# Kernel optimization log

Hardware: AMD Instinct MI355X
Metric: run time of the kernel (lower is better)

Reference implementation:

```python
import jax, jax.numpy as jnp
import numpy as np
import math

EMBED = 1024
HEADS = 16
DHEAD = 64
B, S = 2, 2048


def setup_inputs() -> dict:
    key = jax.random.key(0)
    k1, k2, k3, k4 = jax.random.split(key, 4)
    qs = jax.random.normal(k1, (B, S, EMBED), dtype=jnp.float32)
    # causal mask, broadcast over batch (mask==0 positions are masked out)
    mask = jnp.broadcast_to(jnp.tril(jnp.ones((S, S), dtype=jnp.int32)), (B, S, S))
    # torch Linear(embed, 3*H*D, bias=False): y = x @ W^T; store transposed [E, 3HD]
    Wqkv = jax.random.normal(k2, (EMBED, 3 * HEADS * DHEAD), dtype=jnp.float32) / math.sqrt(EMBED)
    Wout = jax.random.normal(k3, (HEADS * DHEAD, EMBED), dtype=jnp.float32) / math.sqrt(HEADS * DHEAD)
    bout = jax.random.normal(k4, (EMBED,), dtype=jnp.float32) * 0.01
    return {"qs": qs, "mask": mask, "Wqkv": Wqkv, "Wout": Wout, "bout": bout}


def reference(qs, mask, Wqkv, Wout, bout):
    b, s, _ = qs.shape
    # fused QKV projection -> (B, S, 3H, D), split into q/k/v chunks of H heads
    qkv = (qs @ Wqkv).reshape(b, s, 3 * HEADS, DHEAD)
    q, k, v = qkv[:, :, :HEADS], qkv[:, :, HEADS:2 * HEADS], qkv[:, :, 2 * HEADS:]
    # scores: (B, H, Sq, Sk)
    scores = jnp.einsum("bqhd,bkhd->bhqk", q, k) / math.sqrt(DHEAD)
    scores = jnp.where(mask[:, None, :, :] == 0, jnp.float32(-1e9), scores)
    attn = jax.nn.softmax(scores, axis=-1)
    out = jnp.einsum("bhqk,bkhd->bqhd", attn, v).reshape(b, s, HEADS * DHEAD)
    return out @ Wout + bout
```

## Files before the change

kernel.cpp:

```cpp
#include <hip/hip_runtime.h>
#include <hip/hip_bf16.h>
#include <stdint.h>


typedef __attribute__((ext_vector_type(8))) short  short8;
typedef __attribute__((ext_vector_type(4))) short  short4v;
typedef __attribute__((ext_vector_type(4))) float  float4v;

#define SOFTMAX_BIAS 17.3123405f

__device__ __forceinline__ unsigned short f2bf(float f) {
  unsigned int u = __builtin_bit_cast(unsigned int, f);
  u += 0x7fffu + ((u >> 16) & 1u);
  return (unsigned short)(u >> 16);
}
__device__ __forceinline__ unsigned short f2bf_trunc(float f) {
  return (unsigned short)(__builtin_bit_cast(unsigned int, f) >> 16);
}
__device__ __forceinline__ float bf2f(unsigned short s) {
  unsigned int u = ((unsigned int)s) << 16;
  return __builtin_bit_cast(float, u);
}

__device__ __forceinline__ void async_copy16(const void* g, void* l) {
  __builtin_amdgcn_global_load_lds(
      (__attribute__((address_space(1))) unsigned int*)g,
      (__attribute__((address_space(3))) unsigned int*)l, 16, 0, 0);
}

__global__ void prep_kernel(const float* __restrict__ qs,
                            const float* __restrict__ Wqkv,
                            const float* __restrict__ Wout,
                            unsigned short* __restrict__ qs_bf,
                            unsigned short* __restrict__ WqkvT,
                            unsigned short* __restrict__ WoutT) {
  __shared__ float tbuf[32][33];
  const int blk = blockIdx.x, tid = threadIdx.x;
  if (blk < 4096) {
    int i = (blk * 256 + tid) * 4;
    float4v v = *(const float4v*)(qs + i);
    short4v o;
    o[0] = (short)f2bf(v[0]); o[1] = (short)f2bf(v[1]);
    o[2] = (short)f2bf(v[2]); o[3] = (short)f2bf(v[3]);
    *(short4v*)(qs_bf + i) = o;
  } else {
    const float* W; unsigned short* Wt; int N, t;
    if (blk < 4096 + 3072) { W = Wqkv; Wt = WqkvT; N = 3072; t = blk - 4096; }
    else                   { W = Wout; Wt = WoutT; N = 1024; t = blk - 7168; }
    const int tilesx = N >> 5;
    const int n0 = (t % tilesx) * 32, k0 = (t / tilesx) * 32;
    const int x = tid & 31, y = tid >> 5;
#pragma unroll
    for (int i = 0; i < 4; ++i)
      tbuf[y + i * 8][x] = W[(size_t)(k0 + y + i * 8) * N + n0 + x];
    __syncthreads();
#pragma unroll
    for (int i = 0; i < 4; ++i)
      Wt[(size_t)(n0 + y + i * 8) * 1024 + k0 + x] = f2bf(tbuf[x][y + i * 8]);
  }
}

__device__ __forceinline__ void gemm_bt_core(const unsigned short* __restrict__ A,
                                             const unsigned short* __restrict__ Bt,
                                             int m0, int n0,
                                             short* As, short* Bs,
                                             float4v (&acc)[4][4],
                                             int wm, int wn, int l15, int quad,
                                             int tid) {
  for (int k0 = 0; k0 < 1024; k0 += 32) {
    __syncthreads();
#pragma unroll
    for (int i = 0; i < 2; ++i) {
      int u = i * 256 + tid;
      int r = u >> 2, cpw = u & 3;
      int c = cpw ^ ((r >> 1) & 3);
      async_copy16(A  + (size_t)(m0 + r) * 1024 + k0 + c * 8, As + u * 8);
      async_copy16(Bt + (size_t)(n0 + r) * 1024 + k0 + c * 8, Bs + u * 8);
    }
    __syncthreads();

    short8 af[4], bfv[4];
#pragma unroll
    for (int t = 0; t < 4; ++t) {
      int ra = wm * 64 + t * 16 + l15;
      af[t]  = *(const short8*)(As + (ra * 4 + (quad ^ ((ra >> 1) & 3))) * 8);
      int rb = wn * 64 + t * 16 + l15;
      bfv[t] = *(const short8*)(Bs + (rb * 4 + (quad ^ ((rb >> 1) & 3))) * 8);
    }
#pragma unroll
    for (int mt = 0; mt < 4; ++mt)
#pragma unroll
      for (int nt = 0; nt < 4; ++nt)
        acc[mt][nt] = __builtin_amdgcn_mfma_f32_16x16x32_bf16(
            af[mt], bfv[nt], acc[mt][nt], 0, 0, 0);
  }
}

__global__ __launch_bounds__(256, 3)
void gemm_qkv_kernel(const unsigned short* __restrict__ Aq,
                     const unsigned short* __restrict__ Bt,
                     unsigned short* __restrict__ Qb,
                     unsigned short* __restrict__ Kb,
                     unsigned short* __restrict__ Vb) {
  __shared__ short As[128 * 32];
  __shared__ short Bs[128 * 32];
  const int tid = threadIdx.x, lane = tid & 63, w = tid >> 6;
  const int wm = w & 1, wn = w >> 1, l15 = lane & 15, quad = lane >> 4;
  const int m0 = blockIdx.x * 128, n0 = blockIdx.y * 128;

  float4v acc[4][4];
#pragma unroll
  for (int i = 0; i < 4; ++i)
#pragma unroll
    for (int j = 0; j < 4; ++j) acc[i][j] = (float4v)0.0f;

  gemm_bt_core(Aq, Bt, m0, n0, As, Bs, acc, wm, wn, l15, quad, tid);

#pragma unroll
  for (int nt = 0; nt < 4; ++nt) {
    int gn = n0 + wn * 64 + nt * 16 + l15;
    int j = gn >> 6, d = gn & 63;
    int g = j >> 4, h = j & 15;
#pragma unroll
    for (int mt = 0; mt < 4; ++mt) {
#pragma unroll
      for (int r = 0; r < 4; ++r) {
        int gm = m0 + wm * 64 + mt * 16 + quad * 4 + r;
        int b = gm >> 11, s = gm & 2047;
        float v = acc[mt][nt][r];
        if (g == 0)
          Qb[(((size_t)(b * 16 + h) * 2048 + s) << 6) + d] = f2bf(v * 0.18033688f);
        else if (g == 1)
          Kb[(((size_t)(b * 16 + h) * 2048 + s) << 6) + d] = f2bf(v);
        else
          Vb[(((size_t)(b * 16 + h) * 64 + d) << 11) + s] = f2bf(v);
      }
    }
  }
}

__global__ __launch_bounds__(256, 2)
void flash_attn_kernel(const unsigned short* __restrict__ Qb,
                       const unsigned short* __restrict__ Kb,
                       const unsigned short* __restrict__ Vb,
                       unsigned short* __restrict__ Pp0,
                       unsigned short* __restrict__ Pp1,
                       float* __restrict__ lws) {
  __shared__ unsigned short Kt[128 * 64];
  __shared__ unsigned short Vt[64 * 128];
  __shared__ unsigned short Pl[4][32 * 80];

  const int tid = threadIdx.x, lane = tid & 63, w = tid >> 6;
  const int l15 = lane & 15, quad = lane >> 4;
  const int qt = 15 - (blockIdx.x >> 1);
  const int half = blockIdx.x & 1;
  const int bh = blockIdx.y;
  const int bb = bh >> 4, h = bh & 15;

  const int n = qt + 1, nh0 = (n + 1) >> 1;
  const int kt_lo = half ? nh0 : 0;
  const int kt_hi = half ? n : nh0;

  const unsigned short* Qg = Qb + (size_t)bh * 2048 * 64;
  const unsigned short* Kg = Kb + (size_t)bh * 2048 * 64;
  const unsigned short* Vg = Vb + (size_t)bh * 64 * 2048;
  unsigned short* Pw = &Pl[w][0];

  const int qb0 = qt * 128 + w * 32;

  short8 qf[2][2];
#pragma unroll
  for (int nt = 0; nt < 2; ++nt)
#pragma unroll
    for (int kc = 0; kc < 2; ++kc)
      qf[nt][kc] = *(const short8*)(Qg + (size_t)(qb0 + nt * 16 + l15) * 64 +
                                    kc * 32 + quad * 8);

  float l_s[2] = {0.0f, 0.0f};
  float4v o[4][2];
#pragma unroll
  for (int i = 0; i < 4; ++i) { o[i][0] = (float4v)0.0f; o[i][1] = (float4v)0.0f; }

  for (int kt = kt_lo; kt < kt_hi; ++kt) {
    const int kb = kt * 128;
    __syncthreads();
#pragma unroll
    for (int i = 0; i < 4; ++i) {
      int u = i * 256 + tid;
      int r = u >> 3, cp = u & 7;
      async_copy16(Kg + (size_t)(kb + r) * 64 + (cp ^ (r & 7)) * 8, Kt + u * 8);
      int r2 = u >> 4, cp2 = u & 15;
      async_copy16(Vg + (size_t)r2 * 2048 + kb + (cp2 ^ (r2 & 15)) * 8, Vt + u * 8);
    }
    __syncthreads();

    float4v st[8][2];
#pragma unroll
    for (int mt = 0; mt < 8; ++mt) {
      st[mt][0] = (float4v)(-SOFTMAX_BIAS);
      st[mt][1] = (float4v)(-SOFTMAX_BIAS);
      int key = mt * 16 + l15;
#pragma unroll
      for (int kc = 0; kc < 2; ++kc) {
        int cp = (kc * 4 + quad) ^ (key & 7);
        short8 a = *(const short8*)(Kt + key * 64 + cp * 8);
        st[mt][0] = __builtin_amdgcn_mfma_f32_16x16x32_bf16(a, qf[0][kc], st[mt][0], 0, 0, 0);
        st[mt][1] = __builtin_amdgcn_mfma_f32_16x16x32_bf16(a, qf[1][kc], st[mt][1], 0, 0, 0);
      }
    }

    if (kt == qt) {
#pragma unroll
      for (int nt = 0; nt < 2; ++nt) {
        int qg = qb0 + nt * 16 + l15;
#pragma unroll
        for (int mt = 0; mt < 8; ++mt)
#pragma unroll
          for (int r = 0; r < 4; ++r) {
            int keyg = kb + mt * 16 + quad * 4 + r;
            if (keyg > qg) st[mt][nt][r] = -1e5f;
          }
      }
    }

#pragma unroll
    for (int nt = 0; nt < 2; ++nt) {
      float sum = 0.0f;
#pragma unroll
      for (int mt = 0; mt < 8; ++mt)
#pragma unroll
        for (int r = 0; r < 4; ++r) {
          float p = __builtin_amdgcn_exp2f(st[mt][nt][r]);
          st[mt][nt][r] = p;
          sum += p;
        }
      sum += __shfl_xor(sum, 16);
      sum += __shfl_xor(sum, 32);
      l_s[nt] += sum;
    }

#pragma unroll
    for (int hf = 0; hf < 2; ++hf) {
#pragma unroll
      for (int nt = 0; nt < 2; ++nt) {
        int ql = nt * 16 + l15;
        unsigned short* prow = Pw + ql * 80;
#pragma unroll
        for (int mtl = 0; mtl < 4; ++mtl) {
          int mt = hf * 4 + mtl;
          short4v pk;
          pk[0] = (short)f2bf_trunc(st[mt][nt][0]);
          pk[1] = (short)f2bf_trunc(st[mt][nt][1]);
          pk[2] = (short)f2bf_trunc(st[mt][nt][2]);
          pk[3] = (short)f2bf_trunc(st[mt][nt][3]);
          int cp = (mtl * 2 + (quad >> 1)) ^ (l15 & 7);
          *(short4v*)(prow + cp * 8 + (quad & 1) * 4) = pk;
        }
      }
#pragma unroll
      for (int kcl = 0; kcl < 2; ++kcl) {
        int kcg = hf * 2 + kcl;
        short8 pb[2];
#pragma unroll
        for (int nt = 0; nt < 2; ++nt) {
          int ql = nt * 16 + l15;
          int cp = (kcl * 4 + quad) ^ (l15 & 7);
          pb[nt] = *(const short8*)(Pw + ql * 80 + cp * 8);
        }
#pragma unroll
        for (int mtd = 0; mtd < 4; ++mtd) {
          int d = mtd * 16 + l15;
          int cp2 = (kcg * 4 + quad) ^ (d & 15);
          short8 a = *(const short8*)(Vt + d * 128 + cp2 * 8);
          o[mtd][0] = __builtin_amdgcn_mfma_f32_16x16x32_bf16(a, pb[0], o[mtd][0], 0, 0, 0);
          o[mtd][1] = __builtin_amdgcn_mfma_f32_16x16x32_bf16(a, pb[1], o[mtd][1], 0, 0, 0);
        }
      }
    }
  }

  unsigned short* Pp = half ? Pp1 : Pp0;
#pragma unroll
  for (int nt = 0; nt < 2; ++nt) {
    int qg = qb0 + nt * 16 + l15;
    if (quad == 0) lws[half * 65536 + bh * 2048 + qg] = l_s[nt];
#pragma unroll
    for (int mtd = 0; mtd < 4; ++mtd) {
      short4v pk;
      pk[0] = (short)f2bf(o[mtd][nt][0]);
      pk[1] = (short)f2bf(o[mtd][nt][1]);
      pk[2] = (short)f2bf(o[mtd][nt][2]);
      pk[3] = (short)f2bf(o[mtd][nt][3]);
      *(short4v*)(Pp + (size_t)(bb * 2048 + qg) * 1024 + h * 64 + mtd * 16 +
                  quad * 4) = pk;
    }
  }
}

__global__ void combine_kernel(const unsigned short* __restrict__ P0,
                               unsigned short* __restrict__ P1,
                               const float* __restrict__ lws) {
  int idx = (blockIdx.x * 256 + threadIdx.x) * 8;
  int t = idx >> 10, c = idx & 1023;
  int bh = (t >> 11) * 16 + (c >> 6);
  int q = t & 2047;
  float inv = 1.0f / (lws[bh * 2048 + q] + lws[65536 + bh * 2048 + q]);
  short8 a = *(const short8*)(P0 + idx);
  short8 b = *(const short8*)(P1 + idx);
  short8 r;
#pragma unroll
  for (int j = 0; j < 8; ++j)
    r[j] = (short)f2bf((bf2f((unsigned short)a[j]) +
                        bf2f((unsigned short)b[j])) * inv);
  *(short8*)(P1 + idx) = r;
}

__global__ __launch_bounds__(256, 3)
void gemm_out_kernel(const unsigned short* __restrict__ Aq,
                     const unsigned short* __restrict__ Bt,
                     const float* __restrict__ bout,
                     float* __restrict__ out) {
  __shared__ short As[64 * 32];
  __shared__ short Bs[128 * 32];
  const int tid = threadIdx.x, lane = tid & 63, w = tid >> 6;
  const int wm = w & 1, wn = w >> 1, l15 = lane & 15, quad = lane >> 4;
  const int m0 = blockIdx.x * 64, n0 = blockIdx.y * 128;

  float4v acc[2][4];
#pragma unroll
  for (int i = 0; i < 2; ++i)
#pragma unroll
    for (int j = 0; j < 4; ++j) acc[i][j] = (float4v)0.0f;

  for (int k0 = 0; k0 < 1024; k0 += 32) {
    __syncthreads();
    {
      int u = tid;
      int r = u >> 2, cpw = u & 3;
      int c = cpw ^ ((r >> 1) & 3);
      async_copy16(Aq + (size_t)(m0 + r) * 1024 + k0 + c * 8, As + u * 8);
    }
#pragma unroll
    for (int i = 0; i < 2; ++i) {
      int u = i * 256 + tid;
      int r = u >> 2, cpw = u & 3;
      int c = cpw ^ ((r >> 1) & 3);
      async_copy16(Bt + (size_t)(n0 + r) * 1024 + k0 + c * 8, Bs + u * 8);
    }
    __syncthreads();

    short8 af[2], bfv[4];
#pragma unroll
    for (int t = 0; t < 2; ++t) {
      int ra = wm * 32 + t * 16 + l15;
      af[t] = *(const short8*)(As + (ra * 4 + (quad ^ ((ra >> 1) & 3))) * 8);
    }
#pragma unroll
    for (int t = 0; t < 4; ++t) {
      int rb = wn * 64 + t * 16 + l15;
      bfv[t] = *(const short8*)(Bs + (rb * 4 + (quad ^ ((rb >> 1) & 3))) * 8);
    }
#pragma unroll
    for (int mt = 0; mt < 2; ++mt)
#pragma unroll
      for (int nt = 0; nt < 4; ++nt)
        acc[mt][nt] = __builtin_amdgcn_mfma_f32_16x16x32_bf16(
            af[mt], bfv[nt], acc[mt][nt], 0, 0, 0);
  }

#pragma unroll
  for (int nt = 0; nt < 4; ++nt) {
    int gn = n0 + wn * 64 + nt * 16 + l15;
    float bias = bout[gn];
#pragma unroll
    for (int mt = 0; mt < 2; ++mt) {
      int gmb = m0 + wm * 32 + mt * 16 + quad * 4;
#pragma unroll
      for (int r = 0; r < 4; ++r)
        out[(size_t)(gmb + r) * 1024 + gn] = acc[mt][nt][r] + bias;
    }
  }
}

extern "C" void kernel_launch(void* const* d_in, const int* in_sizes, int n_in,
                              void* d_out, int out_size, void* d_ws, size_t ws_size,
                              hipStream_t stream) {
  (void)in_sizes; (void)n_in; (void)out_size; (void)ws_size;
  const float* qs   = (const float*)d_in[0];
  const float* Wqkv = (const float*)d_in[2];
  const float* Wout = (const float*)d_in[3];
  const float* bout = (const float*)d_in[4];
  float* out = (float*)d_out;

  unsigned short* qs_bf = (unsigned short*)d_ws;
  unsigned short* WqkvT = qs_bf + 4096 * 1024;
  unsigned short* WoutT = WqkvT + 3072 * 1024;
  unsigned short* Qb    = WoutT + 1024 * 1024;
  unsigned short* Kb    = Qb + 32 * 2048 * 64;
  unsigned short* Vb    = Kb + 32 * 2048 * 64;
  unsigned short* Ob    = Vb + 32 * 2048 * 64;

  unsigned short* P0 = qs_bf;
  float*          lw = (float*)WqkvT;
  unsigned short* P1 = Ob;

  prep_kernel<<<8192, 256, 0, stream>>>(qs, Wqkv, Wout, qs_bf, WqkvT, WoutT);
  gemm_qkv_kernel<<<dim3(32, 24), 256, 0, stream>>>(qs_bf, WqkvT, Qb, Kb, Vb);
  flash_attn_kernel<<<dim3(32, 32), 256, 0, stream>>>(Qb, Kb, Vb, P0, P1, lw);
  combine_kernel<<<2048, 256, 0, stream>>>(P0, P1, lw);
  gemm_out_kernel<<<dim3(64, 8), 256, 0, stream>>>(P1, WoutT, bout, out);
}
```

Before: 209.4 us.

## Double-buffer K/V tiles in flash attention and shrink P staging buffer

The attention kernel now keeps two LDS buffers for each K and V tile. It prefetches the next key tile asynchronously while the current one is consumed, so the wait on global loads overlaps with MFMA work. The P staging buffer is cut to 32-key chunks, processed in four passes, with a new swizzle. This offsets part of the extra LDS that double buffering costs. The QKV projection epilogue also writes V with packed 4-element stores instead of scalar stores. Together these raise LDS use per block and rely on the top-of-loop barrier to order the async copies.

```diff
diff --git a/kernel.cpp b/kernel.cpp
--- a/kernel.cpp
+++ b/kernel.cpp
@@ -121,19 +121,31 @@
     int gn = n0 + wn * 64 + nt * 16 + l15;
     int j = gn >> 6, d = gn & 63;
     int g = j >> 4, h = j & 15;
-#pragma unroll
-    for (int mt = 0; mt < 4; ++mt) {
-#pragma unroll
-      for (int r = 0; r < 4; ++r) {
-        int gm = m0 + wm * 64 + mt * 16 + quad * 4 + r;
-        int b = gm >> 11, s = gm & 2047;
-        float v = acc[mt][nt][r];
-        if (g == 0)
-          Qb[(((size_t)(b * 16 + h) * 2048 + s) << 6) + d] = f2bf(v * 0.18033688f);
-        else if (g == 1)
-          Kb[(((size_t)(b * 16 + h) * 2048 + s) << 6) + d] = f2bf(v);
-        else
-          Vb[(((size_t)(b * 16 + h) * 64 + d) << 11) + s] = f2bf(v);
+    if (g == 2) {
+#pragma unroll
+      for (int mt = 0; mt < 4; ++mt) {
+        int s0 = m0 + wm * 64 + mt * 16 + quad * 4;
+        int b = s0 >> 11, s = s0 & 2047;
+        short4v pk;
+        pk[0] = (short)f2bf(acc[mt][nt][0]);
+        pk[1] = (short)f2bf(acc[mt][nt][1]);
+        pk[2] = (short)f2bf(acc[mt][nt][2]);
+        pk[3] = (short)f2bf(acc[mt][nt][3]);
+        *(short4v*)(Vb + (((size_t)(b * 16 + h) * 64 + d) << 11) + s) = pk;
+      }
+    } else {
+#pragma unroll
+      for (int mt = 0; mt < 4; ++mt) {
+#pragma unroll
+        for (int r = 0; r < 4; ++r) {
+          int gm = m0 + wm * 64 + mt * 16 + quad * 4 + r;
+          int b = gm >> 11, s = gm & 2047;
+          float v = acc[mt][nt][r];
+          if (g == 0)
+            Qb[(((size_t)(b * 16 + h) * 2048 + s) << 6) + d] = f2bf(v * 0.18033688f);
+          else
+            Kb[(((size_t)(b * 16 + h) * 2048 + s) << 6) + d] = f2bf(v);
+        }
       }
     }
   }
@@ -146,9 +158,9 @@
                        unsigned short* __restrict__ Pp0,
                        unsigned short* __restrict__ Pp1,
                        float* __restrict__ lws) {
-  __shared__ unsigned short Kt[128 * 64];
-  __shared__ unsigned short Vt[64 * 128];
-  __shared__ unsigned short Pl[4][32 * 80];
+  __shared__ unsigned short Kt[2][128 * 64];
+  __shared__ unsigned short Vt[2][64 * 128];
+  __shared__ unsigned short Pl[4][32 * 36];
 
   const int tid = threadIdx.x, lane = tid & 63, w = tid >> 6;
   const int l15 = lane & 15, quad = lane >> 4;
@@ -168,6 +180,8 @@
 
   const int qb0 = qt * 128 + w * 32;
 
+  const int uK[4] = {tid, 256 + tid, 512 + tid, 768 + tid};
+
   short8 qf[2][2];
 #pragma unroll
   for (int nt = 0; nt < 2; ++nt)
@@ -181,18 +195,40 @@
 #pragma unroll
   for (int i = 0; i < 4; ++i) { o[i][0] = (float4v)0.0f; o[i][1] = (float4v)0.0f; }
 
-  for (int kt = kt_lo; kt < kt_hi; ++kt) {
+#pragma unroll
+  for (int i = 0; i < 4; ++i) {
+    int u = uK[i];
+    int r = u >> 3, cp = u & 7;
+    async_copy16(Kg + (size_t)(kt_lo * 128 + r) * 64 + (cp ^ (r & 7)) * 8,
+                 &Kt[0][0] + u * 8);
+    int r2 = u >> 4, cp2 = u & 15;
+    async_copy16(Vg + (size_t)r2 * 2048 + kt_lo * 128 + (cp2 ^ (r2 & 15)) * 8,
+                 &Vt[0][0] + u * 8);
+  }
+
+  int buf = 0;
+  for (int kt = kt_lo; kt < kt_hi; ++kt, buf ^= 1) {
     const int kb = kt * 128;
     __syncthreads();
-#pragma unroll
-    for (int i = 0; i < 4; ++i) {
-      int u = i * 256 + tid;
-      int r = u >> 3, cp = u & 7;
-      async_copy16(Kg + (size_t)(kb + r) * 64 + (cp ^ (r & 7)) * 8, Kt + u * 8);
-      int r2 = u >> 4, cp2 = u & 15;
-      async_copy16(Vg + (size_t)r2 * 2048 + kb + (cp2 ^ (r2 & 15)) * 8, Vt + u * 8);
-    }
-    __syncthreads();
+
+    if (kt + 1 < kt_hi) {
+      const int kb2 = kb + 128;
+      const unsigned short* Kd = &Kt[buf ^ 1][0];
+      const unsigned short* Vd = &Vt[buf ^ 1][0];
+#pragma unroll
+      for (int i = 0; i < 4; ++i) {
+        int u = uK[i];
+        int r = u >> 3, cp = u & 7;
+        async_copy16(Kg + (size_t)(kb2 + r) * 64 + (cp ^ (r & 7)) * 8,
+                     (void*)(Kd + u * 8));
+        int r2 = u >> 4, cp2 = u & 15;
+        async_copy16(Vg + (size_t)r2 * 2048 + kb2 + (cp2 ^ (r2 & 15)) * 8,
+                     (void*)(Vd + u * 8));
+      }
+    }
+
+    const unsigned short* Kc = &Kt[buf][0];
+    const unsigned short* Vc = &Vt[buf][0];
 
     float4v st[8][2];
 #pragma unroll
@@ -203,7 +239,7 @@
 #pragma unroll
       for (int kc = 0; kc < 2; ++kc) {
         int cp = (kc * 4 + quad) ^ (key & 7);
-        short8 a = *(const short8*)(Kt + key * 64 + cp * 8);
+        short8 a = *(const short8*)(Kc + key * 64 + cp * 8);
         st[mt][0] = __builtin_amdgcn_mfma_f32_16x16x32_bf16(a, qf[0][kc], st[mt][0], 0, 0, 0);
         st[mt][1] = __builtin_amdgcn_mfma_f32_16x16x32_bf16(a, qf[1][kc], st[mt][1], 0, 0, 0);
       }
@@ -240,41 +276,37 @@
     }
 
 #pragma unroll
-    for (int hf = 0; hf < 2; ++hf) {
+    for (int qr = 0; qr < 4; ++qr) {
 #pragma unroll
       for (int nt = 0; nt < 2; ++nt) {
         int ql = nt * 16 + l15;
-        unsigned short* prow = Pw + ql * 80;
-#pragma unroll
-        for (int mtl = 0; mtl < 4; ++mtl) {
-          int mt = hf * 4 + mtl;
+        unsigned short* prow = Pw + ql * 36;
+#pragma unroll
+        for (int mtl = 0; mtl < 2; ++mtl) {
+          int mt = qr * 2 + mtl;
           short4v pk;
           pk[0] = (short)f2bf_trunc(st[mt][nt][0]);
           pk[1] = (short)f2bf_trunc(st[mt][nt][1]);
           pk[2] = (short)f2bf_trunc(st[mt][nt][2]);
           pk[3] = (short)f2bf_trunc(st[mt][nt][3]);
-          int cp = (mtl * 2 + (quad >> 1)) ^ (l15 & 7);
+          int cp = (mtl * 2 + (quad >> 1)) ^ (ql & 3);
           *(short4v*)(prow + cp * 8 + (quad & 1) * 4) = pk;
         }
       }
-#pragma unroll
-      for (int kcl = 0; kcl < 2; ++kcl) {
-        int kcg = hf * 2 + kcl;
-        short8 pb[2];
-#pragma unroll
-        for (int nt = 0; nt < 2; ++nt) {
-          int ql = nt * 16 + l15;
-          int cp = (kcl * 4 + quad) ^ (l15 & 7);
-          pb[nt] = *(const short8*)(Pw + ql * 80 + cp * 8);
-        }
-#pragma unroll
-        for (int mtd = 0; mtd < 4; ++mtd) {
-          int d = mtd * 16 + l15;
-          int cp2 = (kcg * 4 + quad) ^ (d & 15);
-          short8 a = *(const short8*)(Vt + d * 128 + cp2 * 8);
-          o[mtd][0] = __builtin_amdgcn_mfma_f32_16x16x32_bf16(a, pb[0], o[mtd][0], 0, 0, 0);
-          o[mtd][1] = __builtin_amdgcn_mfma_f32_16x16x32_bf16(a, pb[1], o[mtd][1], 0, 0, 0);
-        }
+      short8 pb[2];
+#pragma unroll
+      for (int nt = 0; nt < 2; ++nt) {
+        int ql = nt * 16 + l15;
+        int cp = quad ^ (ql & 3);
+        pb[nt] = *(const short8*)(Pw + ql * 36 + cp * 8);
+      }
+#pragma unroll
+      for (int mtd = 0; mtd < 4; ++mtd) {
+        int d = mtd * 16 + l15;
+        int cp2 = (qr * 4 + quad) ^ (d & 15);
+        short8 a = *(const short8*)(Vc + d * 128 + cp2 * 8);
+        o[mtd][0] = __builtin_amdgcn_mfma_f32_16x16x32_bf16(a, pb[0], o[mtd][0], 0, 0, 0);
+        o[mtd][1] = __builtin_amdgcn_mfma_f32_16x16x32_bf16(a, pb[1], o[mtd][1], 0, 0, 0);
       }
     }
   }
```

Result: slower. 221.9 us (+6.0%).

## Store V row-major via transposed QKV GEMM and read V columns in attention

Applied to the files above, without the earlier changes.

The QKV GEMM's operands are swapped so it computes the transposed product (W^T X^T). Each lane can then write 4 contiguous bf16 head-dim values for Q, K and V, replacing scalar scattered stores, including the strided transposed V store. V is kept in the same [token, d] layout as K. The attention kernel loads V tiles with a rotation swizzle and gathers its MFMA A-operand with 8 scalar LDS reads per fragment. The P staging buffer is shrunk and the attention kernel's occupancy hint is raised from 2 to 3 blocks. The trade is cheaper, coalesced GEMM epilogue stores against many more LDS read instructions in the attention inner loop.

```diff
diff --git a/kernel.cpp b/kernel.cpp
--- a/kernel.cpp
+++ b/kernel.cpp
@@ -8,6 +8,7 @@
 typedef __attribute__((ext_vector_type(4))) float  float4v;
 
 #define SOFTMAX_BIAS 17.3123405f
+#define QSCALE 0.18033688f
 
 __device__ __forceinline__ unsigned short f2bf(float f) {
   unsigned int u = __builtin_bit_cast(unsigned int, f);
@@ -97,8 +98,8 @@
 }
 
 __global__ __launch_bounds__(256, 3)
-void gemm_qkv_kernel(const unsigned short* __restrict__ Aq,
-                     const unsigned short* __restrict__ Bt,
+void gemm_qkv_kernel(const unsigned short* __restrict__ Wt,
+                     const unsigned short* __restrict__ Xt,
                      unsigned short* __restrict__ Qb,
                      unsigned short* __restrict__ Kb,
                      unsigned short* __restrict__ Vb) {
@@ -114,32 +115,31 @@
 #pragma unroll
     for (int j = 0; j < 4; ++j) acc[i][j] = (float4v)0.0f;
 
-  gemm_bt_core(Aq, Bt, m0, n0, As, Bs, acc, wm, wn, l15, quad, tid);
-
-#pragma unroll
-  for (int nt = 0; nt < 4; ++nt) {
-    int gn = n0 + wn * 64 + nt * 16 + l15;
-    int j = gn >> 6, d = gn & 63;
+  gemm_bt_core(Wt, Xt, m0, n0, As, Bs, acc, wm, wn, l15, quad, tid);
+
+#pragma unroll
+  for (int mt = 0; mt < 4; ++mt) {
+    int gnb = m0 + wm * 64 + mt * 16;
+    int j = gnb >> 6, d0 = gnb & 63;
     int g = j >> 4, h = j & 15;
-#pragma unroll
-    for (int mt = 0; mt < 4; ++mt) {
-#pragma unroll
-      for (int r = 0; r < 4; ++r) {
-        int gm = m0 + wm * 64 + mt * 16 + quad * 4 + r;
-        int b = gm >> 11, s = gm & 2047;
-        float v = acc[mt][nt][r];
-        if (g == 0)
-          Qb[(((size_t)(b * 16 + h) * 2048 + s) << 6) + d] = f2bf(v * 0.18033688f);
-        else if (g == 1)
-          Kb[(((size_t)(b * 16 + h) * 2048 + s) << 6) + d] = f2bf(v);
-        else
-          Vb[(((size_t)(b * 16 + h) * 64 + d) << 11) + s] = f2bf(v);
-      }
-    }
-  }
-}
-
-__global__ __launch_bounds__(256, 2)
+    unsigned short* base = (g == 0) ? Qb : (g == 1) ? Kb : Vb;
+    float sc = (g == 0) ? QSCALE : 1.0f;
+#pragma unroll
+    for (int nt = 0; nt < 4; ++nt) {
+      int token = n0 + wn * 64 + nt * 16 + l15;
+      int b = token >> 11, s = token & 2047;
+      short4v pk;
+      pk[0] = (short)f2bf(acc[mt][nt][0] * sc);
+      pk[1] = (short)f2bf(acc[mt][nt][1] * sc);
+      pk[2] = (short)f2bf(acc[mt][nt][2] * sc);
+      pk[3] = (short)f2bf(acc[mt][nt][3] * sc);
+      *(short4v*)(base + (((size_t)(b * 16 + h) * 2048 + s) << 6) +
+                  d0 + quad * 4) = pk;
+    }
+  }
+}
+
+__global__ __launch_bounds__(256, 3)
 void flash_attn_kernel(const unsigned short* __restrict__ Qb,
                        const unsigned short* __restrict__ Kb,
                        const unsigned short* __restrict__ Vb,
@@ -147,8 +147,8 @@
                        unsigned short* __restrict__ Pp1,
                        float* __restrict__ lws) {
   __shared__ unsigned short Kt[128 * 64];
-  __shared__ unsigned short Vt[64 * 128];
-  __shared__ unsigned short Pl[4][32 * 80];
+  __shared__ unsigned short Vt[128 * 64];
+  __shared__ unsigned short Pl[4][32 * 36];
 
   const int tid = threadIdx.x, lane = tid & 63, w = tid >> 6;
   const int l15 = lane & 15, quad = lane >> 4;
@@ -163,7 +163,7 @@
 
   const unsigned short* Qg = Qb + (size_t)bh * 2048 * 64;
   const unsigned short* Kg = Kb + (size_t)bh * 2048 * 64;
-  const unsigned short* Vg = Vb + (size_t)bh * 64 * 2048;
+  const unsigned short* Vg = Vb + (size_t)bh * 2048 * 64;
   unsigned short* Pw = &Pl[w][0];
 
   const int qb0 = qt * 128 + w * 32;
@@ -189,8 +189,8 @@
       int u = i * 256 + tid;
       int r = u >> 3, cp = u & 7;
       async_copy16(Kg + (size_t)(kb + r) * 64 + (cp ^ (r & 7)) * 8, Kt + u * 8);
-      int r2 = u >> 4, cp2 = u & 15;
-      async_copy16(Vg + (size_t)r2 * 2048 + kb + (cp2 ^ (r2 & 15)) * 8, Vt + u * 8);
+      int rot = ((r >> 3) & 3) << 4;
+      async_copy16(Vg + (size_t)(kb + r) * 64 + ((cp * 8 - rot) & 63), Vt + u * 8);
     }
     __syncthreads();
 
@@ -240,41 +240,40 @@
     }
 
 #pragma unroll
-    for (int hf = 0; hf < 2; ++hf) {
+    for (int qr = 0; qr < 4; ++qr) {
 #pragma unroll
       for (int nt = 0; nt < 2; ++nt) {
         int ql = nt * 16 + l15;
-        unsigned short* prow = Pw + ql * 80;
-#pragma unroll
-        for (int mtl = 0; mtl < 4; ++mtl) {
-          int mt = hf * 4 + mtl;
+        unsigned short* prow = Pw + ql * 36;
+#pragma unroll
+        for (int mtl = 0; mtl < 2; ++mtl) {
+          int mt = qr * 2 + mtl;
           short4v pk;
           pk[0] = (short)f2bf_trunc(st[mt][nt][0]);
           pk[1] = (short)f2bf_trunc(st[mt][nt][1]);
           pk[2] = (short)f2bf_trunc(st[mt][nt][2]);
           pk[3] = (short)f2bf_trunc(st[mt][nt][3]);
-          int cp = (mtl * 2 + (quad >> 1)) ^ (l15 & 7);
+          int cp = (mtl * 2 + (quad >> 1)) ^ (ql & 3);
           *(short4v*)(prow + cp * 8 + (quad & 1) * 4) = pk;
         }
       }
-#pragma unroll
-      for (int kcl = 0; kcl < 2; ++kcl) {
-        int kcg = hf * 2 + kcl;
-        short8 pb[2];
-#pragma unroll
-        for (int nt = 0; nt < 2; ++nt) {
-          int ql = nt * 16 + l15;
-          int cp = (kcl * 4 + quad) ^ (l15 & 7);
-          pb[nt] = *(const short8*)(Pw + ql * 80 + cp * 8);
-        }
-#pragma unroll
-        for (int mtd = 0; mtd < 4; ++mtd) {
-          int d = mtd * 16 + l15;
-          int cp2 = (kcg * 4 + quad) ^ (d & 15);
-          short8 a = *(const short8*)(Vt + d * 128 + cp2 * 8);
-          o[mtd][0] = __builtin_amdgcn_mfma_f32_16x16x32_bf16(a, pb[0], o[mtd][0], 0, 0, 0);
-          o[mtd][1] = __builtin_amdgcn_mfma_f32_16x16x32_bf16(a, pb[1], o[mtd][1], 0, 0, 0);
-        }
+      short8 pb[2];
+#pragma unroll
+      for (int nt = 0; nt < 2; ++nt) {
+        int ql = nt * 16 + l15;
+        int cp = quad ^ (ql & 3);
+        pb[nt] = *(const short8*)(Pw + ql * 36 + cp * 8);
+      }
+#pragma unroll
+      for (int mtd = 0; mtd < 4; ++mtd) {
+        int d = mtd * 16 + l15;
+        int dd = (d + (quad << 4)) & 63;
+        const unsigned short* vrow = Vt + (size_t)(qr * 32 + quad * 8) * 64 + dd;
+        short8 a;
+#pragma unroll
+        for (int jj = 0; jj < 8; ++jj) a[jj] = (short)vrow[jj * 64];
+        o[mtd][0] = __builtin_amdgcn_mfma_f32_16x16x32_bf16(a, pb[0], o[mtd][0], 0, 0, 0);
+        o[mtd][1] = __builtin_amdgcn_mfma_f32_16x16x32_bf16(a, pb[1], o[mtd][1], 0, 0, 0);
       }
     }
   }
@@ -405,7 +404,7 @@
   unsigned short* P1 = Ob;
 
   prep_kernel<<<8192, 256, 0, stream>>>(qs, Wqkv, Wout, qs_bf, WqkvT, WoutT);
-  gemm_qkv_kernel<<<dim3(32, 24), 256, 0, stream>>>(qs_bf, WqkvT, Qb, Kb, Vb);
+  gemm_qkv_kernel<<<dim3(24, 32), 256, 0, stream>>>(WqkvT, qs_bf, Qb, Kb, Vb);
   flash_attn_kernel<<<dim3(32, 32), 256, 0, stream>>>(Qb, Kb, Vb, P0, P1, lw);
   combine_kernel<<<2048, 256, 0, stream>>>(P0, P1, lw);
   gemm_out_kernel<<<dim3(64, 8), 256, 0, stream>>>(P1, WoutT, bout, out);
```

New measurement: 262.8 us. 25.5% more time.

## Shrink P staging buffer, defer row-sum reduction, vectorize V stores, raise occupancy

Applied to the files above, without the earlier changes.

The flash attention kernel now stages P through LDS in four 32-key chunks with a smaller per-wave buffer, which cuts LDS use and allows three blocks per CU via launch bounds. The per-iteration cross-lane shuffle reduction of the softmax row sum is moved to a single reduction after the key loop. The QKV projection epilogue writes transposed V as packed 4-element vectors instead of scalar stores. The tighter register budget from the higher occupancy target risks spills, and the extra LDS write/read rounds may add sync-free latency.

```diff
diff --git a/kernel.cpp b/kernel.cpp
--- a/kernel.cpp
+++ b/kernel.cpp
@@ -8,6 +8,7 @@
 typedef __attribute__((ext_vector_type(4))) float  float4v;
 
 #define SOFTMAX_BIAS 17.3123405f
+#define QSCALE 0.18033688f
 
 __device__ __forceinline__ unsigned short f2bf(float f) {
   unsigned int u = __builtin_bit_cast(unsigned int, f);
@@ -121,25 +122,37 @@
     int gn = n0 + wn * 64 + nt * 16 + l15;
     int j = gn >> 6, d = gn & 63;
     int g = j >> 4, h = j & 15;
-#pragma unroll
-    for (int mt = 0; mt < 4; ++mt) {
-#pragma unroll
-      for (int r = 0; r < 4; ++r) {
-        int gm = m0 + wm * 64 + mt * 16 + quad * 4 + r;
-        int b = gm >> 11, s = gm & 2047;
-        float v = acc[mt][nt][r];
-        if (g == 0)
-          Qb[(((size_t)(b * 16 + h) * 2048 + s) << 6) + d] = f2bf(v * 0.18033688f);
-        else if (g == 1)
-          Kb[(((size_t)(b * 16 + h) * 2048 + s) << 6) + d] = f2bf(v);
-        else
-          Vb[(((size_t)(b * 16 + h) * 64 + d) << 11) + s] = f2bf(v);
-      }
-    }
-  }
-}
-
-__global__ __launch_bounds__(256, 2)
+    if (g == 2) {
+#pragma unroll
+      for (int mt = 0; mt < 4; ++mt) {
+        int s0 = m0 + wm * 64 + mt * 16 + quad * 4;
+        int b = s0 >> 11, s = s0 & 2047;
+        short4v pk;
+        pk[0] = (short)f2bf(acc[mt][nt][0]);
+        pk[1] = (short)f2bf(acc[mt][nt][1]);
+        pk[2] = (short)f2bf(acc[mt][nt][2]);
+        pk[3] = (short)f2bf(acc[mt][nt][3]);
+        *(short4v*)(Vb + (((size_t)(b * 16 + h) * 64 + d) << 11) + s) = pk;
+      }
+    } else {
+#pragma unroll
+      for (int mt = 0; mt < 4; ++mt) {
+#pragma unroll
+        for (int r = 0; r < 4; ++r) {
+          int gm = m0 + wm * 64 + mt * 16 + quad * 4 + r;
+          int b = gm >> 11, s = gm & 2047;
+          float v = acc[mt][nt][r];
+          if (g == 0)
+            Qb[(((size_t)(b * 16 + h) * 2048 + s) << 6) + d] = f2bf(v * QSCALE);
+          else
+            Kb[(((size_t)(b * 16 + h) * 2048 + s) << 6) + d] = f2bf(v);
+        }
+      }
+    }
+  }
+}
+
+__global__ __launch_bounds__(256, 3)
 void flash_attn_kernel(const unsigned short* __restrict__ Qb,
                        const unsigned short* __restrict__ Kb,
                        const unsigned short* __restrict__ Vb,
@@ -148,7 +161,7 @@
                        float* __restrict__ lws) {
   __shared__ unsigned short Kt[128 * 64];
   __shared__ unsigned short Vt[64 * 128];
-  __shared__ unsigned short Pl[4][32 * 80];
+  __shared__ unsigned short Pl[4][32 * 36];
 
   const int tid = threadIdx.x, lane = tid & 63, w = tid >> 6;
   const int l15 = lane & 15, quad = lane >> 4;
@@ -234,47 +247,41 @@
           st[mt][nt][r] = p;
           sum += p;
         }
-      sum += __shfl_xor(sum, 16);
-      sum += __shfl_xor(sum, 32);
       l_s[nt] += sum;
     }
 
 #pragma unroll
-    for (int hf = 0; hf < 2; ++hf) {
+    for (int qr = 0; qr < 4; ++qr) {
 #pragma unroll
       for (int nt = 0; nt < 2; ++nt) {
         int ql = nt * 16 + l15;
-        unsigned short* prow = Pw + ql * 80;
-#pragma unroll
-        for (int mtl = 0; mtl < 4; ++mtl) {
-          int mt = hf * 4 + mtl;
+        unsigned short* prow = Pw + ql * 36;
+#pragma unroll
+        for (int mtl = 0; mtl < 2; ++mtl) {
+          int mt = qr * 2 + mtl;
           short4v pk;
           pk[0] = (short)f2bf_trunc(st[mt][nt][0]);
           pk[1] = (short)f2bf_trunc(st[mt][nt][1]);
           pk[2] = (short)f2bf_trunc(st[mt][nt][2]);
           pk[3] = (short)f2bf_trunc(st[mt][nt][3]);
-          int cp = (mtl * 2 + (quad >> 1)) ^ (l15 & 7);
+          int cp = (mtl * 2 + (quad >> 1)) ^ (ql & 3);
           *(short4v*)(prow + cp * 8 + (quad & 1) * 4) = pk;
         }
       }
-#pragma unroll
-      for (int kcl = 0; kcl < 2; ++kcl) {
-        int kcg = hf * 2 + kcl;
-        short8 pb[2];
-#pragma unroll
-        for (int nt = 0; nt < 2; ++nt) {
-          int ql = nt * 16 + l15;
-          int cp = (kcl * 4 + quad) ^ (l15 & 7);
-          pb[nt] = *(const short8*)(Pw + ql * 80 + cp * 8);
-        }
-#pragma unroll
-        for (int mtd = 0; mtd < 4; ++mtd) {
-          int d = mtd * 16 + l15;
-          int cp2 = (kcg * 4 + quad) ^ (d & 15);
-          short8 a = *(const short8*)(Vt + d * 128 + cp2 * 8);
-          o[mtd][0] = __builtin_amdgcn_mfma_f32_16x16x32_bf16(a, pb[0], o[mtd][0], 0, 0, 0);
-          o[mtd][1] = __builtin_amdgcn_mfma_f32_16x16x32_bf16(a, pb[1], o[mtd][1], 0, 0, 0);
-        }
+      short8 pb[2];
+#pragma unroll
+      for (int nt = 0; nt < 2; ++nt) {
+        int ql = nt * 16 + l15;
+        int cp = quad ^ (ql & 3);
+        pb[nt] = *(const short8*)(Pw + ql * 36 + cp * 8);
+      }
+#pragma unroll
+      for (int mtd = 0; mtd < 4; ++mtd) {
+        int d = mtd * 16 + l15;
+        int cp2 = (qr * 4 + quad) ^ (d & 15);
+        short8 a = *(const short8*)(Vt + d * 128 + cp2 * 8);
+        o[mtd][0] = __builtin_amdgcn_mfma_f32_16x16x32_bf16(a, pb[0], o[mtd][0], 0, 0, 0);
+        o[mtd][1] = __builtin_amdgcn_mfma_f32_16x16x32_bf16(a, pb[1], o[mtd][1], 0, 0, 0);
       }
     }
   }
@@ -282,8 +289,11 @@
   unsigned short* Pp = half ? Pp1 : Pp0;
 #pragma unroll
   for (int nt = 0; nt < 2; ++nt) {
+    float l = l_s[nt];
+    l += __shfl_xor(l, 16);
+    l += __shfl_xor(l, 32);
     int qg = qb0 + nt * 16 + l15;
-    if (quad == 0) lws[half * 65536 + bh * 2048 + qg] = l_s[nt];
+    if (quad == 0) lws[half * 65536 + bh * 2048 + qg] = l;
 #pragma unroll
     for (int mtd = 0; mtd < 4; ++mtd) {
       short4v pk;
```

Result: slower. 278.7 us (+33.1%).
